# Kernel optimization log

Hardware: AMD Instinct MI355X
Metric: run time of the kernel (lower is better)

The kernel has to match this reference:

```python
import jax, jax.numpy as jnp
import numpy as np

B, H, S = 256, 128, 2048

def setup_inputs() -> dict:
    key = jax.random.key(0)
    ks = jax.random.split(key, 8)
    static_embedding = jax.random.normal(ks[0], (B, H, S), dtype=jnp.float32)
    dynamic_embedding = jax.random.normal(ks[1], (B, S, H), dtype=jnp.float32)
    decoder_output = jax.random.normal(ks[2], (B, H, 1), dtype=jnp.float32)
    mask = jax.random.randint(ks[3], (B, S), 0, 2).astype(bool)
    # xavier-uniform-ish init scales
    lim_v = float(np.sqrt(6.0 / (1 + H)))
    lim_W = float(np.sqrt(6.0 / (H + 3 * H)))
    lim_W2 = float(np.sqrt(6.0 / (H + 2 * H)))
    v = jax.random.uniform(ks[4], (H,), minval=-lim_v, maxval=lim_v, dtype=jnp.float32)
    W = jax.random.uniform(ks[5], (H, 3 * H), minval=-lim_W, maxval=lim_W, dtype=jnp.float32)
    v2 = jax.random.uniform(ks[6], (H,), minval=-lim_v, maxval=lim_v, dtype=jnp.float32)
    W2 = jax.random.uniform(ks[7], (H, 2 * H), minval=-lim_W2, maxval=lim_W2, dtype=jnp.float32)
    return {"static_embedding": static_embedding, "dynamic_embedding": dynamic_embedding,
            "decoder_output": decoder_output, "mask": mask,
            "v": v, "W": W, "v2": v2, "W2": W2}


def reference(static_embedding, dynamic_embedding, decoder_output, mask, v, W, v2, W2):
    b, h, s = static_embedding.shape
    dec = jnp.broadcast_to(decoder_output, (b, h, s))               # [B,H,S]
    hidden = jnp.concatenate(
        [static_embedding, jnp.swapaxes(dynamic_embedding, 1, 2), dec], axis=1)  # [B,3H,S]
    # stage 1: additive scoring  v^T tanh(W @ hidden)
    t1 = jnp.tanh(jnp.einsum('hk,bks->bhs', W, hidden))             # [B,H,S]
    attns = jnp.einsum('h,bhs->bs', v, t1)                          # [B,S]
    enc_attn = jax.nn.softmax(attns, axis=1)                        # [B,S]
    # context over static embeddings
    context = jnp.einsum('bs,bhs->bh', enc_attn, static_embedding)  # [B,H]
    energy = jnp.concatenate(
        [static_embedding, jnp.broadcast_to(context[:, :, None], (b, h, s))], axis=1)  # [B,2H,S]
    # stage 2
    t2 = jnp.tanh(jnp.einsum('hk,bks->bhs', W2, energy))            # [B,H,S]
    probs = jnp.einsum('h,bhs->bs', v2, t2)                         # [B,S]
    probs = jnp.where(mask, -jnp.inf, probs)
    return jax.nn.softmax(probs, axis=1)
```

## Files before the change

### kernel.cpp

```cpp
#include <hip/hip_runtime.h>
#include <stdint.h>
#include <math.h>

#define B_ 256
#define H_ 128
#define S_ 2048

typedef __attribute__((ext_vector_type(8))) short short8;
typedef __attribute__((ext_vector_type(4))) float f32x4;
typedef __attribute__((ext_vector_type(4))) unsigned int u32x4;

typedef const __attribute__((address_space(1))) void gvoid_t;
typedef __attribute__((address_space(3))) void lvoid_t;

__device__ __forceinline__ unsigned short f2bf(float f) {
  uint32_t u = __builtin_bit_cast(uint32_t, f);
  u += 0x7fffu + ((u >> 16) & 1u);
  return (unsigned short)(u >> 16);
}

__device__ __forceinline__ uint32_t cvtpk(float lo, float hi) {
  uint32_t r;
  asm("v_cvt_pk_bf16_f32 %0, %1, %2" : "=v"(r) : "v"(lo), "v"(hi));
  return r;
}

__device__ __forceinline__ float bf2f(unsigned short u) {
  return __builtin_bit_cast(float, (uint32_t)u << 16);
}

__device__ __forceinline__ float tanh5(float x) {
  float e = __builtin_amdgcn_exp2f(x * 2.8853900817779268f);
  float r = __builtin_amdgcn_rcpf(1.0f + e);
  return fmaf(-2.0f, r, 1.0f);
}

#define WS_NEED 4718592u
#define WST_OFF 8388608u
#define WS_T_NEED (WST_OFF + (size_t)B_ * (S_/16) * 4 * 64 * 8 * 2)

__global__ __launch_bounds__(256) void prep_wfrags(
    const float* __restrict__ W, const float* __restrict__ W2,
    unsigned short* __restrict__ wsA) {
  int idx = blockIdx.x * 256 + threadIdx.x;
  if (idx >= 24 * 4 * 64 * 8) return;
  int j = idx & 7;
  int lane = (idx >> 3) & 63;
  int t = (idx >> 9) & 3;
  int tile = idx >> 11;
  int li = lane & 15;
  int k = t * 32 + (lane >> 4) * 8 + j;
  float val;
  if (tile < 8)        val = W[(tile * 16 + li) * 384 + k];
  else if (tile < 16)  val = W2[((tile - 8) * 16 + li) * 256 + k];
  else                 val = W[((tile - 16) * 16 + li) * 384 + 128 + k];
  wsA[idx] = f2bf(val);
}

__global__ __launch_bounds__(128) void prep_c1(
    const float* __restrict__ W, const float* __restrict__ dec,
    float* __restrict__ c1) {
  int b = blockIdx.x;
  int h = threadIdx.x;
  __shared__ float sdec[H_];
  sdec[h] = dec[b * H_ + h];
  __syncthreads();
  const float* wr = W + h * 384 + 256;
  float acc = 0.f;
  #pragma unroll 4
  for (int k = 0; k < 128; ++k) acc += wr[k] * sdec[k];
  c1[b * H_ + h] = acc;
}

__global__ void detect_mask(const unsigned char* __restrict__ mb, int* __restrict__ flag) {
  __shared__ int sGT1, sNZ;
  if (threadIdx.x == 0) { sGT1 = 0; sNZ = 0; }
  __syncthreads();
  int gt1 = 0, nz = 0;
  for (int i = threadIdx.x; i < 8192; i += 256) {
    unsigned char c = mb[i];
    if (c > 1) gt1 = 1;
    if ((i & 3) && c) nz = 1;
  }
  if (gt1) atomicOr(&sGT1, 1);
  if (nz)  atomicOr(&sNZ, 1);
  __syncthreads();
  if (threadIdx.x == 0) *flag = sGT1 ? 2 : (sNZ ? 1 : 0);
}

__global__ __launch_bounds__(256) void stage1(
    const float* __restrict__ sEmb, const float* __restrict__ dEmb,
    const unsigned short* __restrict__ wsA, const float* __restrict__ c1,
    const float* __restrict__ v, float* __restrict__ attns,
    unsigned short* __restrict__ wsT) {
  const int b = blockIdx.y;
  const int tid = threadIdx.x;
  const int lane = tid & 63, w = tid >> 6, g = lane >> 4, li = lane & 15;
  __shared__ float sS[128 * 64];
  __shared__ unsigned short frag[4][8][512];
  __shared__ float spart[256];
  __shared__ float sc1[H_], sv[H_];

  const size_t sbase = (size_t)b * H_ * S_;
  const size_t dbase = (size_t)b * S_ * H_;
  const int sblk = blockIdx.x * 512;

  short8 aW[2][4], aB[2][4];
  #pragma unroll
  for (int mm = 0; mm < 2; ++mm)
    #pragma unroll
    for (int t = 0; t < 4; ++t) {
      aW[mm][t] = *(const short8*)(wsA + (size_t)(((2 * w + mm) * 4 + t) * 64 + lane) * 8);
      aB[mm][t] = *(const short8*)(wsA + (size_t)(((16 + 2 * w + mm) * 4 + t) * 64 + lane) * 8);
    }
  if (tid < 128) { sc1[tid] = c1[b * H_ + tid]; sv[tid] = v[tid]; }

  const int lrow = lane >> 4, lcol4 = 4 * (lane & 15);
  auto stageS = [&](int soff) {
    #pragma unroll
    for (int i = 0; i < 8; ++i) {
      int r = 32 * w + 4 * i + lrow;
      int gcol = lcol4 ^ (((r >> 3) & 3) << 3);
      const float* src = sEmb + sbase + (size_t)r * S_ + soff + gcol;
      __builtin_amdgcn_global_load_lds((gvoid_t*)src, (lvoid_t*)&sS[(32 * w + 4 * i) * 64],
                                       16, 0, 0);
    }
  };
  f32x4 dv[8];
  auto loadD = [&](int soff) {
    const float* dr = dEmb + dbase + (size_t)(soff + 16 * w + li) * H_ + 8 * g;
    #pragma unroll
    for (int t = 0; t < 4; ++t) {
      dv[2 * t]     = *(const f32x4*)(dr + 32 * t);
      dv[2 * t + 1] = *(const f32x4*)(dr + 32 * t + 4);
    }
  };

  stageS(sblk);
  loadD(sblk);

  const int colA = (16 * w + li) ^ (g << 3);

  for (int c = 0; c < 8; ++c) {
    const int soff = sblk + c * 64;
    __syncthreads();
    if (c > 0 && tid < 64)
      attns[(size_t)b * S_ + soff - 64 + tid] =
          spart[tid] + spart[64 + tid] + spart[128 + tid] + spart[192 + tid];

    #pragma unroll
    for (int t = 0; t < 4; ++t) {
      const int rb = (32 * t + 8 * g) * 64 + colA;
      uint32_t s0 = cvtpk(sS[rb], sS[rb + 64]);
      uint32_t s1 = cvtpk(sS[rb + 128], sS[rb + 192]);
      uint32_t s2 = cvtpk(sS[rb + 256], sS[rb + 320]);
      uint32_t s3 = cvtpk(sS[rb + 384], sS[rb + 448]);
      u32x4 us = {s0, s1, s2, s3};
      short8 bS = __builtin_bit_cast(short8, us);
      uint32_t d0 = cvtpk(dv[2 * t].x, dv[2 * t].y);
      uint32_t d1 = cvtpk(dv[2 * t].z, dv[2 * t].w);
      uint32_t d2 = cvtpk(dv[2 * t + 1].x, dv[2 * t + 1].y);
      uint32_t d3 = cvtpk(dv[2 * t + 1].z, dv[2 * t + 1].w);
      u32x4 ud = {d0, d1, d2, d3};
      short8 bD = __builtin_bit_cast(short8, ud);
      *(short8*)&frag[w][t][lane * 8] = bS;
      *(short8*)&frag[w][4 + t][lane * 8] = bD;
      if (wsT)
        *(short8*)&wsT[(((size_t)b * (S_ / 16) + (soff >> 4) + w) * 4 + t) * 512 + lane * 8] = bS;
    }
    __syncthreads();
    if (c + 1 < 8) { stageS(soff + 64); loadD(soff + 64); }

    f32x4 acc[4][2];
    #pragma unroll
    for (int st = 0; st < 4; ++st) { acc[st][0] = (f32x4)0.0f; acc[st][1] = (f32x4)0.0f; }
    #pragma unroll
    for (int st = 0; st < 4; ++st)
      #pragma unroll
      for (int t = 0; t < 4; ++t) {
        short8 bS = *(const short8*)&frag[st][t][lane * 8];
        short8 bD = *(const short8*)&frag[st][4 + t][lane * 8];
        acc[st][0] = __builtin_amdgcn_mfma_f32_16x16x32_bf16(aW[0][t], bS, acc[st][0], 0, 0, 0);
        acc[st][1] = __builtin_amdgcn_mfma_f32_16x16x32_bf16(aW[1][t], bS, acc[st][1], 0, 0, 0);
        acc[st][0] = __builtin_amdgcn_mfma_f32_16x16x32_bf16(aB[0][t], bD, acc[st][0], 0, 0, 0);
        acc[st][1] = __builtin_amdgcn_mfma_f32_16x16x32_bf16(aB[1][t], bD, acc[st][1], 0, 0, 0);
      }

    #pragma unroll
    for (int st = 0; st < 4; ++st) {
      float part = 0.f;
      #pragma unroll
      for (int mm = 0; mm < 2; ++mm)
        #pragma unroll
        for (int r = 0; r < 4; ++r) {
          int h = 32 * w + 16 * mm + 4 * g + r;
          part += sv[h] * tanh5(acc[st][mm][r] + sc1[h]);
        }
      part += __shfl_xor(part, 16);
      part += __shfl_xor(part, 32);
      if (lane < 16) spart[w * 64 + st * 16 + li] = part;
    }
  }
  __syncthreads();
  if (tid < 64)
    attns[(size_t)b * S_ + sblk + 448 + tid] =
        spart[tid] + spart[64 + tid] + spart[128 + tid] + spart[192 + tid];
}

__global__ __launch_bounds__(512) void fuse2(
    const float* __restrict__ attns, const unsigned short* __restrict__ wsT,
    const unsigned short* __restrict__ wsA, const float* __restrict__ W2,
    const float* __restrict__ v2, const unsigned char* __restrict__ mask8,
    const int* __restrict__ flag, float* __restrict__ out) {
  const int b = blockIdx.x;
  const int tid = threadIdx.x;
  const int lane = tid & 63, wv = tid >> 6, g = lane >> 4, li = lane & 15;
  __shared__ float buf[S_];
  __shared__ float sctx[8][H_];
  __shared__ float2 sq[H_];
  __shared__ float wred[8];
  __shared__ float sred;

  const size_t pbase = (size_t)b * (S_ / 16);

  float a[4];
  #pragma unroll
  for (int i = 0; i < 4; ++i) a[i] = attns[(size_t)b * S_ + i * 512 + tid];
  float mx = fmaxf(fmaxf(a[0], a[1]), fmaxf(a[2], a[3]));
  #pragma unroll
  for (int off = 32; off >= 1; off >>= 1) mx = fmaxf(mx, __shfl_xor(mx, off));
  if (lane == 0) wred[wv] = mx;
  __syncthreads();
  if (tid == 0) {
    float m = wred[0];
    #pragma unroll
    for (int i = 1; i < 8; ++i) m = fmaxf(m, wred[i]);
    sred = m;
  }
  __syncthreads();
  mx = sred;
  __syncthreads();
  float sum = 0.f;
  #pragma unroll
  for (int i = 0; i < 4; ++i) {
    float e = __expf(a[i] - mx);
    buf[i * 512 + tid] = e;
    sum += e;
  }
  #pragma unroll
  for (int off = 32; off >= 1; off >>= 1) sum += __shfl_xor(sum, off);
  if (lane == 0) wred[wv] = sum;
  __syncthreads();
  if (tid == 0) {
    float s = 0.f;
    #pragma unroll
    for (int i = 0; i < 8; ++i) s += wred[i];
    sred = 1.0f / s;
  }
  __syncthreads();
  const float inv1 = sred;
  __syncthreads();

  float hacc[4][8];
  #pragma unroll
  for (int t = 0; t < 4; ++t)
    #pragma unroll
    for (int j = 0; j < 8; ++j) hacc[t][j] = 0.f;
  short8 cur[4];
  #pragma unroll
  for (int t = 0; t < 4; ++t)
    cur[t] = *(const short8*)&wsT[((pbase + wv) * 4 + t) * 512 + lane * 8];
  for (int stile = wv; stile < 128; stile += 8) {
    short8 nxt[4];
    const bool more = (stile + 8) < 128;
    if (more) {
      #pragma unroll
      for (int t = 0; t < 4; ++t)
        nxt[t] = *(const short8*)&wsT[((pbase + stile + 8) * 4 + t) * 512 + lane * 8];
    }
    float pw = buf[stile * 16 + li];
    #pragma unroll
    for (int t = 0; t < 4; ++t)
      #pragma unroll
      for (int j = 0; j < 8; ++j)
        hacc[t][j] = fmaf(pw, bf2f((unsigned short)cur[t][j]), hacc[t][j]);
    if (more) {
      #pragma unroll
      for (int t = 0; t < 4; ++t) cur[t] = nxt[t];
    }
  }
  #pragma unroll
  for (int t = 0; t < 4; ++t)
    #pragma unroll
    for (int j = 0; j < 8; ++j) {
      float x = hacc[t][j];
      x += __shfl_xor(x, 1); x += __shfl_xor(x, 2);
      x += __shfl_xor(x, 4); x += __shfl_xor(x, 8);
      hacc[t][j] = x;
    }
  if (li == 0) {
    #pragma unroll
    for (int t = 0; t < 4; ++t)
      #pragma unroll
      for (int j = 0; j < 8; ++j)
        sctx[wv][32 * t + 8 * g + j] = hacc[t][j];
  }
  __syncthreads();

  if (tid < 128) {
    float cx = 0.f;
    #pragma unroll
    for (int q = 0; q < 8; ++q) cx += sctx[q][tid];
    sctx[0][tid] = cx * inv1;
  }
  __syncthreads();
  if (tid < 128) {
    const float* wr = W2 + tid * 256 + 128;
    float c2v = 0.f;
    #pragma unroll 4
    for (int k = 0; k < 128; ++k) c2v += wr[k] * sctx[0][k];
    sq[tid] = make_float2(c2v, v2[tid]);
  }
  __syncthreads();

  short8 aW[8][4];
  #pragma unroll
  for (int m = 0; m < 8; ++m)
    #pragma unroll
    for (int t = 0; t < 4; ++t)
      aW[m][t] = *(const short8*)(wsA + (size_t)(((8 + m) * 4 + t) * 64 + lane) * 8);
  const int f = *flag;

  short8 bcur[4];
  #pragma unroll
  for (int t = 0; t < 4; ++t)
    bcur[t] = *(const short8*)&wsT[((pbase + wv) * 4 + t) * 512 + lane * 8];
  for (int stile = wv; stile < 128; stile += 8) {
    short8 bnxt[4];
    const bool more = (stile + 8) < 128;
    if (more) {
      #pragma unroll
      for (int t = 0; t < 4; ++t)
        bnxt[t] = *(const short8*)&wsT[((pbase + stile + 8) * 4 + t) * 512 + lane * 8];
    }
    f32x4 acc[8];
    #pragma unroll
    for (int m = 0; m < 8; ++m) acc[m] = (f32x4)0.0f;
    #pragma unroll
    for (int t = 0; t < 4; ++t)
      #pragma unroll
      for (int m = 0; m < 8; ++m)
        acc[m] = __builtin_amdgcn_mfma_f32_16x16x32_bf16(aW[m][t], bcur[t], acc[m], 0, 0, 0);
    float part = 0.f;
    #pragma unroll
    for (int m = 0; m < 8; ++m)
      #pragma unroll
      for (int r = 0; r < 4; ++r) {
        float2 q = sq[16 * m + 4 * g + r];
        part += q.y * tanh5(acc[m][r] + q.x);
      }
    part += __shfl_xor(part, 16);
    part += __shfl_xor(part, 32);
    if (lane < 16) {
      int s = stile * 16 + li;
      size_t mi = (size_t)b * S_ + s;
      bool msk;
      if (f == 1)      msk = mask8[mi] != 0;
      else if (f == 2) msk = ((const float*)mask8)[mi] != 0.0f;
      else             msk = ((const int*)mask8)[mi] != 0;
      buf[s] = msk ? -INFINITY : part;
    }
    if (more) {
      #pragma unroll
      for (int t = 0; t < 4; ++t) bcur[t] = bnxt[t];
    }
  }
  __syncthreads();

  float s4[4];
  #pragma unroll
  for (int i = 0; i < 4; ++i) s4[i] = buf[i * 512 + tid];
  float mx2 = fmaxf(fmaxf(s4[0], s4[1]), fmaxf(s4[2], s4[3]));
  #pragma unroll
  for (int off = 32; off >= 1; off >>= 1) mx2 = fmaxf(mx2, __shfl_xor(mx2, off));
  if (lane == 0) wred[wv] = mx2;
  __syncthreads();
  if (tid == 0) {
    float m = wred[0];
    #pragma unroll
    for (int i = 1; i < 8; ++i) m = fmaxf(m, wred[i]);
    sred = m;
  }
  __syncthreads();
  mx2 = sred;
  __syncthreads();
  float e4[4];
  float sum2 = 0.f;
  #pragma unroll
  for (int i = 0; i < 4; ++i) { e4[i] = __expf(s4[i] - mx2); sum2 += e4[i]; }
  #pragma unroll
  for (int off = 32; off >= 1; off >>= 1) sum2 += __shfl_xor(sum2, off);
  if (lane == 0) wred[wv] = sum2;
  __syncthreads();
  if (tid == 0) {
    float s = 0.f;
    #pragma unroll
    for (int i = 0; i < 8; ++i) s += wred[i];
    sred = 1.0f / s;
  }
  __syncthreads();
  const float inv2 = sred;
  #pragma unroll
  for (int i = 0; i < 4; ++i) out[(size_t)b * S_ + i * 512 + tid] = e4[i] * inv2;
}

__global__ __launch_bounds__(256) void kmid_a(
    const float* __restrict__ attns, const float* __restrict__ sEmb,
    float* __restrict__ ctx) {
  int q = blockIdx.x, b = blockIdx.y;
  int tid = threadIdx.x, lane = tid & 63, w = tid >> 6;
  __shared__ float p[S_];
  __shared__ float wred[4];
  __shared__ float sred;
  float a[8];
  #pragma unroll
  for (int i = 0; i < 8; ++i) a[i] = attns[(size_t)b * S_ + i * 256 + tid];
  float mx = a[0];
  #pragma unroll
  for (int i = 1; i < 8; ++i) mx = fmaxf(mx, a[i]);
  #pragma unroll
  for (int off = 32; off >= 1; off >>= 1) mx = fmaxf(mx, __shfl_xor(mx, off));
  if (lane == 0) wred[w] = mx;
  __syncthreads();
  if (tid == 0) sred = fmaxf(fmaxf(wred[0], wred[1]), fmaxf(wred[2], wred[3]));
  __syncthreads();
  mx = sred;
  __syncthreads();
  float sum = 0.f;
  #pragma unroll
  for (int i = 0; i < 8; ++i) {
    float e = __expf(a[i] - mx);
    p[i * 256 + tid] = e;
    sum += e;
  }
  #pragma unroll
  for (int off = 32; off >= 1; off >>= 1) sum += __shfl_xor(sum, off);
  if (lane == 0) wred[w] = sum;
  __syncthreads();
  if (tid == 0) sred = 1.0f / (wred[0] + wred[1] + wred[2] + wred[3]);
  __syncthreads();
  float inv = sred;
  #pragma unroll
  for (int hh = 0; hh < 8; ++hh) {
    int h = q * 32 + w * 8 + hh;
    const f32x4* xp = (const f32x4*)(sEmb + (size_t)b * H_ * S_ + (size_t)h * S_);
    float av = 0.f;
    #pragma unroll
    for (int it = 0; it < 8; ++it) {
      f32x4 x = xp[it * 64 + lane];
      f32x4 pp = *(const f32x4*)&p[(it * 64 + lane) * 4];
      av += x.x * pp.x + x.y * pp.y + x.z * pp.z + x.w * pp.w;
    }
    #pragma unroll
    for (int off = 32; off >= 1; off >>= 1) av += __shfl_xor(av, off);
    if (lane == 0) ctx[b * H_ + h] = av * inv;
  }
}

__global__ __launch_bounds__(128) void kmid_b(
    const float* __restrict__ W2, const float* __restrict__ ctx,
    float* __restrict__ c2) {
  int b = blockIdx.x;
  int h = threadIdx.x;
  __shared__ float sc[H_];
  sc[h] = ctx[b * H_ + h];
  __syncthreads();
  const float* wr = W2 + h * 256 + 128;
  float acc = 0.f;
  #pragma unroll 4
  for (int k = 0; k < 128; ++k) acc += wr[k] * sc[k];
  c2[b * H_ + h] = acc;
}

__global__ __launch_bounds__(256) void stage2F(
    const float* __restrict__ sEmb, const unsigned short* __restrict__ wsA,
    const float* __restrict__ c2, const float* __restrict__ v2,
    const unsigned char* __restrict__ mask8, const int* __restrict__ flag,
    float* __restrict__ score) {
  int b = blockIdx.y;
  int tid = threadIdx.x;
  int lane = tid & 63, w = tid >> 6, g = lane >> 4, li = lane & 15;
  __shared__ float sS[128 * 64];
  __shared__ float sc2[H_], sv2[H_];
  __shared__ float spart[256];
  const int schunk = blockIdx.x * 64;
  const size_t sbase = (size_t)b * H_ * S_;
  short8 aW[2][4];
  #pragma unroll
  for (int mm = 0; mm < 2; ++mm)
    #pragma unroll
    for (int t = 0; t < 4; ++t)
      aW[mm][t] = *(const short8*)(wsA + (size_t)(((8 + 2 * w + mm) * 4 + t) * 64 + lane) * 8);
  {
    int lrow = lane >> 4, lcol4 = 4 * (lane & 15);
    #pragma unroll
    for (int i = 0; i < 8; ++i) {
      int r = 32 * w + 4 * i + lrow;
      int gcol = lcol4 ^ (((r >> 3) & 3) << 3);
      const float* src = sEmb + sbase + (size_t)r * S_ + schunk + gcol;
      __builtin_amdgcn_global_load_lds((gvoid_t*)src, (lvoid_t*)&sS[(32 * w + 4 * i) * 64],
                                       16, 0, 0);
    }
  }
  if (tid < 128) { sc2[tid] = c2[b * H_ + tid]; sv2[tid] = v2[tid]; }
  __syncthreads();
  f32x4 acc[4][2];
  #pragma unroll
  for (int st = 0; st < 4; ++st) { acc[st][0] = (f32x4)0.0f; acc[st][1] = (f32x4)0.0f; }
  #pragma unroll
  for (int st = 0; st < 4; ++st) {
    const int colA = (16 * st + li) ^ (g << 3);
    #pragma unroll
    for (int t = 0; t < 4; ++t) {
      short8 bS;
      #pragma unroll
      for (int j = 0; j < 8; ++j)
        bS[j] = (short)f2bf(sS[(32 * t + 8 * g + j) * 64 + colA]);
      acc[st][0] = __builtin_amdgcn_mfma_f32_16x16x32_bf16(aW[0][t], bS, acc[st][0], 0, 0, 0);
      acc[st][1] = __builtin_amdgcn_mfma_f32_16x16x32_bf16(aW[1][t], bS, acc[st][1], 0, 0, 0);
    }
  }
  #pragma unroll
  for (int st = 0; st < 4; ++st) {
    float part = 0.f;
    #pragma unroll
    for (int mm = 0; mm < 2; ++mm)
      #pragma unroll
      for (int r = 0; r < 4; ++r) {
        int h = 32 * w + 16 * mm + 4 * g + r;
        part += sv2[h] * tanh5(acc[st][mm][r] + sc2[h]);
      }
    part += __shfl_xor(part, 16);
    part += __shfl_xor(part, 32);
    if (lane < 16) spart[w * 64 + st * 16 + li] = part;
  }
  __syncthreads();
  if (tid < 64) {
    float tot = spart[tid] + spart[64 + tid] + spart[128 + tid] + spart[192 + tid];
    size_t mi = (size_t)b * S_ + schunk + tid;
    int f = *flag;
    bool msk;
    if (f == 1)      msk = mask8[mi] != 0;
    else if (f == 2) msk = ((const float*)mask8)[mi] != 0.0f;
    else             msk = ((const int*)mask8)[mi] != 0;
    score[mi] = msk ? -INFINITY : tot;
  }
}

__global__ __launch_bounds__(256) void ksoftmax(
    const float* __restrict__ score, float* __restrict__ out) {
  int b = blockIdx.x;
  int tid = threadIdx.x, lane = tid & 63, w = tid >> 6;
  __shared__ float wred[4];
  __shared__ float sred;
  float a[8];
  #pragma unroll
  for (int i = 0; i < 8; ++i) a[i] = score[(size_t)b * S_ + i * 256 + tid];
  float mx = a[0];
  #pragma unroll
  for (int i = 1; i < 8; ++i) mx = fmaxf(mx, a[i]);
  #pragma unroll
  for (int off = 32; off >= 1; off >>= 1) mx = fmaxf(mx, __shfl_xor(mx, off));
  if (lane == 0) wred[w] = mx;
  __syncthreads();
  if (tid == 0) sred = fmaxf(fmaxf(wred[0], wred[1]), fmaxf(wred[2], wred[3]));
  __syncthreads();
  mx = sred;
  __syncthreads();
  float e[8];
  float sum = 0.f;
  #pragma unroll
  for (int i = 0; i < 8; ++i) { e[i] = __expf(a[i] - mx); sum += e[i]; }
  #pragma unroll
  for (int off = 32; off >= 1; off >>= 1) sum += __shfl_xor(sum, off);
  if (lane == 0) wred[w] = sum;
  __syncthreads();
  if (tid == 0) sred = 1.0f / (wred[0] + wred[1] + wred[2] + wred[3]);
  __syncthreads();
  float inv = sred;
  #pragma unroll
  for (int i = 0; i < 8; ++i) out[(size_t)b * S_ + i * 256 + tid] = e[i] * inv;
}

extern "C" void kernel_launch(void* const* d_in, const int* in_sizes, int n_in,
                              void* d_out, int out_size, void* d_ws, size_t ws_size,
                              hipStream_t stream) {
  (void)in_sizes; (void)n_in; (void)out_size;
  if (ws_size < WS_NEED) return;
  const float* sEmb = (const float*)d_in[0];
  const float* dEmb = (const float*)d_in[1];
  const float* dec  = (const float*)d_in[2];
  const unsigned char* mask = (const unsigned char*)d_in[3];
  const float* v    = (const float*)d_in[4];
  const float* W    = (const float*)d_in[5];
  const float* v2   = (const float*)d_in[6];
  const float* W2   = (const float*)d_in[7];

  char* ws = (char*)d_ws;
  unsigned short* wsA = (unsigned short*)(ws);
  int*   flag  = (int*)  (ws + 114688);
  float* c1    = (float*)(ws + 131072);
  float* c2    = (float*)(ws + 262144);
  float* ctx   = (float*)(ws + 393216);
  float* attns = (float*)(ws + 524288);
  float* score = (float*)(ws + 2621440);
  bool useT = (ws_size >= WS_T_NEED);
  unsigned short* wsT = useT ? (unsigned short*)(ws + WST_OFF) : nullptr;

  prep_wfrags<<<192, 256, 0, stream>>>(W, W2, wsA);
  prep_c1<<<B_, 128, 0, stream>>>(W, dec, c1);
  detect_mask<<<1, 256, 0, stream>>>(mask, flag);
  stage1<<<dim3(4, B_), 256, 0, stream>>>(sEmb, dEmb, wsA, c1, v, attns, wsT);
  if (useT) {
    fuse2<<<B_, 512, 0, stream>>>(attns, wsT, wsA, W2, v2, mask, flag, (float*)d_out);
  } else {
    kmid_a<<<dim3(4, B_), 256, 0, stream>>>(attns, sEmb, ctx);
    kmid_b<<<B_, 128, 0, stream>>>(W2, ctx, c2);
    stage2F<<<dim3(32, B_), 256, 0, stream>>>(sEmb, wsA, c2, v2, mask, flag, score);
    ksoftmax<<<B_, 256, 0, stream>>>(score, (float*)d_out);
  }
}
```

Measured before the change: 229.9 us.

## Double-buffer stage1 with 32-column chunks, manual waitcnt and more blocks

Rewrites stage1 for the workspace path so each block covers 256 columns in 32-column chunks with double-buffered LDS staging and prefetch two chunks ahead. Explicit vmcnt/lgkmcnt waits and sched barriers control overlap, the grid doubles to 8×B, and launch bounds request 3 blocks per CU. The aim is to hide HBM latency behind MFMA work and raise occupancy. The old kernel is kept as a fallback without the wsT store, and the hand-tuned wait counts are fragile if the compiler changes how many memory instructions it issues.

```diff
diff --git a/kernel.cpp b/kernel.cpp
--- a/kernel.cpp
+++ b/kernel.cpp
@@ -12,6 +12,8 @@
 
 typedef const __attribute__((address_space(1))) void gvoid_t;
 typedef __attribute__((address_space(3))) void lvoid_t;
+
+#define SCHED0 __builtin_amdgcn_sched_barrier(0)
 
 __device__ __forceinline__ unsigned short f2bf(float f) {
   uint32_t u = __builtin_bit_cast(uint32_t, f);
@@ -88,7 +90,9 @@
   if (threadIdx.x == 0) *flag = sGT1 ? 2 : (sNZ ? 1 : 0);
 }
 
-__global__ __launch_bounds__(256) void stage1(
+struct D4 { f32x4 v[4]; };
+
+__global__ __launch_bounds__(256, 3) void stage1(
     const float* __restrict__ sEmb, const float* __restrict__ dEmb,
     const unsigned short* __restrict__ wsA, const float* __restrict__ c1,
     const float* __restrict__ v, float* __restrict__ attns,
@@ -96,6 +100,376 @@
   const int b = blockIdx.y;
   const int tid = threadIdx.x;
   const int lane = tid & 63, w = tid >> 6, g = lane >> 4, li = lane & 15;
+  const int stl = w >> 1, tp = w & 1;
+  __shared__ float sS[2][128 * 32];
+  __shared__ unsigned short frag[2][8][512];
+  __shared__ float spart[4][32];
+  __shared__ float sc1[H_], sv[H_];
+
+  const size_t sbase = (size_t)b * H_ * S_;
+  const size_t dbase = (size_t)b * S_ * H_;
+  const int sblk = blockIdx.x * 256;
+  const int CHUNKS = 8;
+
+  short8 aW[2][4], aB[2][4];
+  #pragma unroll
+  for (int mm = 0; mm < 2; ++mm)
+    #pragma unroll
+    for (int t = 0; t < 4; ++t) {
+      aW[mm][t] = *(const short8*)(wsA + (size_t)(((2 * w + mm) * 4 + t) * 64 + lane) * 8);
+      aB[mm][t] = *(const short8*)(wsA + (size_t)(((16 + 2 * w + mm) * 4 + t) * 64 + lane) * 8);
+    }
+  {
+    int hh = 32 * w + (lane & 31);
+    sc1[hh] = c1[b * H_ + hh];
+    sv[hh]  = v[hh];
+  }
+
+  auto stageS = [&](int soff2, int buf) {
+    #pragma unroll
+    for (int i = 0; i < 4; ++i) {
+      int rr = 32 * w + 8 * i + (lane >> 3);
+      int gcol = (4 * (lane & 7)) ^ (i << 3);
+      const float* src = sEmb + sbase + (size_t)rr * S_ + soff2 + gcol;
+      __builtin_amdgcn_global_load_lds((gvoid_t*)src,
+                                       (lvoid_t*)&sS[buf][(32 * w + 8 * i) * 32], 16, 0, 0);
+    }
+  };
+  auto loadD = [&](int soff2) -> D4 {
+    D4 r;
+    const float* dr = dEmb + dbase + (size_t)(soff2 + 16 * stl + li) * H_ + 64 * tp + 8 * g;
+    r.v[0] = *(const f32x4*)(dr);
+    r.v[1] = *(const f32x4*)(dr + 4);
+    r.v[2] = *(const f32x4*)(dr + 32);
+    r.v[3] = *(const f32x4*)(dr + 36);
+    return r;
+  };
+
+  SCHED0;
+  stageS(sblk, 0);
+  SCHED0;
+  D4 dvA = loadD(sblk);
+  SCHED0;
+  stageS(sblk + 32, 1);
+  SCHED0;
+  D4 dvB = loadD(sblk + 32);
+  SCHED0;
+
+  const int colr = (16 * stl + li) ^ (g << 3);
+
+  for (int c = 0; c < CHUNKS; ++c) {
+    const int soff = sblk + c * 32;
+
+    if (c == 0)                 { asm volatile("s_waitcnt vmcnt(8)" ::: "memory"); }
+    else if (c == 1)            { asm volatile("s_waitcnt vmcnt(10)" ::: "memory"); }
+    else if (c == CHUNKS - 1)   { asm volatile("s_waitcnt vmcnt(3)" ::: "memory"); }
+    else                        { asm volatile("s_waitcnt vmcnt(11)" ::: "memory"); }
+    asm volatile("s_waitcnt lgkmcnt(0)" ::: "memory");
+    SCHED0;
+    __builtin_amdgcn_s_barrier();
+    SCHED0;
+
+    if (c > 0) {
+      int idx = 8 * w + (lane & 7);
+      float tot = spart[0][idx] + spart[1][idx] + spart[2][idx] + spart[3][idx];
+      if (lane < 8) attns[(size_t)b * S_ + soff - 32 + idx] = tot;
+    }
+
+    {
+      const float* sSc = sS[c & 1];
+      const f32x4* dvv = (c & 1) ? dvB.v : dvA.v;
+      #pragma unroll
+      for (int tt = 0; tt < 2; ++tt) {
+        const int t = 2 * tp + tt;
+        const int rb = (32 * t + 8 * g) * 32 + colr;
+        uint32_t s0 = cvtpk(sSc[rb], sSc[rb + 32]);
+        uint32_t s1 = cvtpk(sSc[rb + 64], sSc[rb + 96]);
+        uint32_t s2 = cvtpk(sSc[rb + 128], sSc[rb + 160]);
+        uint32_t s3 = cvtpk(sSc[rb + 192], sSc[rb + 224]);
+        u32x4 us = {s0, s1, s2, s3};
+        short8 bS = __builtin_bit_cast(short8, us);
+        f32x4 a0 = dvv[2 * tt], a1 = dvv[2 * tt + 1];
+        uint32_t d0 = cvtpk(a0.x, a0.y);
+        uint32_t d1 = cvtpk(a0.z, a0.w);
+        uint32_t d2 = cvtpk(a1.x, a1.y);
+        uint32_t d3 = cvtpk(a1.z, a1.w);
+        u32x4 ud = {d0, d1, d2, d3};
+        short8 bD = __builtin_bit_cast(short8, ud);
+        *(short8*)&frag[stl][t][lane * 8] = bS;
+        *(short8*)&frag[stl][4 + t][lane * 8] = bD;
+        *(short8*)&wsT[(((size_t)b * (S_ / 16) + (soff >> 4) + stl) * 4 + t) * 512 + lane * 8] = bS;
+      }
+    }
+
+    asm volatile("s_waitcnt lgkmcnt(0)" ::: "memory");
+    SCHED0;
+    __builtin_amdgcn_s_barrier();
+    SCHED0;
+
+    if (c + 2 < CHUNKS) {
+      stageS(soff + 64, c & 1);
+      SCHED0;
+      if ((c & 1) == 0) dvA = loadD(soff + 64);
+      else              dvB = loadD(soff + 64);
+    }
+    SCHED0;
+
+    f32x4 acc[2][2];
+    #pragma unroll
+    for (int st = 0; st < 2; ++st) { acc[st][0] = (f32x4)0.0f; acc[st][1] = (f32x4)0.0f; }
+    #pragma unroll
+    for (int st = 0; st < 2; ++st)
+      #pragma unroll
+      for (int t = 0; t < 4; ++t) {
+        short8 bS = *(const short8*)&frag[st][t][lane * 8];
+        short8 bD = *(const short8*)&frag[st][4 + t][lane * 8];
+        acc[st][0] = __builtin_amdgcn_mfma_f32_16x16x32_bf16(aW[0][t], bS, acc[st][0], 0, 0, 0);
+        acc[st][1] = __builtin_amdgcn_mfma_f32_16x16x32_bf16(aW[1][t], bS, acc[st][1], 0, 0, 0);
+        acc[st][0] = __builtin_amdgcn_mfma_f32_16x16x32_bf16(aB[0][t], bD, acc[st][0], 0, 0, 0);
+        acc[st][1] = __builtin_amdgcn_mfma_f32_16x16x32_bf16(aB[1][t], bD, acc[st][1], 0, 0, 0);
+      }
+
+    #pragma unroll
+    for (int st = 0; st < 2; ++st) {
+      float part = 0.f;
+      #pragma unroll
+      for (int mm = 0; mm < 2; ++mm)
+        #pragma unroll
+        for (int r = 0; r < 4; ++r) {
+          int h = 32 * w + 16 * mm + 4 * g + r;
+          part += sv[h] * tanh5(acc[st][mm][r] + sc1[h]);
+        }
+      part += __shfl_xor(part, 16);
+      part += __shfl_xor(part, 32);
+      if (lane < 16) spart[w][16 * st + li] = part;
+    }
+  }
+
+  asm volatile("s_waitcnt lgkmcnt(0)" ::: "memory");
+  SCHED0;
+  __builtin_amdgcn_s_barrier();
+  SCHED0;
+  {
+    int idx = 8 * w + (lane & 7);
+    float tot = spart[0][idx] + spart[1][idx] + spart[2][idx] + spart[3][idx];
+    if (lane < 8) attns[(size_t)b * S_ + sblk + (CHUNKS - 1) * 32 + idx] = tot;
+  }
+}
+
+__global__ __launch_bounds__(512) void fuse2(
+    const float* __restrict__ attns, const unsigned short* __restrict__ wsT,
+    const unsigned short* __restrict__ wsA, const float* __restrict__ W2,
+    const float* __restrict__ v2, const unsigned char* __restrict__ mask8,
+    const int* __restrict__ flag, float* __restrict__ out) {
+  const int b = blockIdx.x;
+  const int tid = threadIdx.x;
+  const int lane = tid & 63, wv = tid >> 6, g = lane >> 4, li = lane & 15;
+  __shared__ float buf[S_];
+  __shared__ float sctx[8][H_];
+  __shared__ float2 sq[H_];
+  __shared__ float wred[8];
+  __shared__ float sred;
+
+  const size_t pbase = (size_t)b * (S_ / 16);
+
+  float a[4];
+  #pragma unroll
+  for (int i = 0; i < 4; ++i) a[i] = attns[(size_t)b * S_ + i * 512 + tid];
+  float mx = fmaxf(fmaxf(a[0], a[1]), fmaxf(a[2], a[3]));
+  #pragma unroll
+  for (int off = 32; off >= 1; off >>= 1) mx = fmaxf(mx, __shfl_xor(mx, off));
+  if (lane == 0) wred[wv] = mx;
+  __syncthreads();
+  if (tid == 0) {
+    float m = wred[0];
+    #pragma unroll
+    for (int i = 1; i < 8; ++i) m = fmaxf(m, wred[i]);
+    sred = m;
+  }
+  __syncthreads();
+  mx = sred;
+  __syncthreads();
+  float sum = 0.f;
+  #pragma unroll
+  for (int i = 0; i < 4; ++i) {
+    float e = __expf(a[i] - mx);
+    buf[i * 512 + tid] = e;
+    sum += e;
+  }
+  #pragma unroll
+  for (int off = 32; off >= 1; off >>= 1) sum += __shfl_xor(sum, off);
+  if (lane == 0) wred[wv] = sum;
+  __syncthreads();
+  if (tid == 0) {
+    float s = 0.f;
+    #pragma unroll
+    for (int i = 0; i < 8; ++i) s += wred[i];
+    sred = 1.0f / s;
+  }
+  __syncthreads();
+  const float inv1 = sred;
+  __syncthreads();
+
+  float hacc[4][8];
+  #pragma unroll
+  for (int t = 0; t < 4; ++t)
+    #pragma unroll
+    for (int j = 0; j < 8; ++j) hacc[t][j] = 0.f;
+  short8 cur[4];
+  #pragma unroll
+  for (int t = 0; t < 4; ++t)
+    cur[t] = *(const short8*)&wsT[((pbase + wv) * 4 + t) * 512 + lane * 8];
+  for (int stile = wv; stile < 128; stile += 8) {
+    short8 nxt[4];
+    const bool more = (stile + 8) < 128;
+    if (more) {
+      #pragma unroll
+      for (int t = 0; t < 4; ++t)
+        nxt[t] = *(const short8*)&wsT[((pbase + stile + 8) * 4 + t) * 512 + lane * 8];
+    }
+    float pw = buf[stile * 16 + li];
+    #pragma unroll
+    for (int t = 0; t < 4; ++t)
+      #pragma unroll
+      for (int j = 0; j < 8; ++j)
+        hacc[t][j] = fmaf(pw, bf2f((unsigned short)cur[t][j]), hacc[t][j]);
+    if (more) {
+      #pragma unroll
+      for (int t = 0; t < 4; ++t) cur[t] = nxt[t];
+    }
+  }
+  #pragma unroll
+  for (int t = 0; t < 4; ++t)
+    #pragma unroll
+    for (int j = 0; j < 8; ++j) {
+      float x = hacc[t][j];
+      x += __shfl_xor(x, 1); x += __shfl_xor(x, 2);
+      x += __shfl_xor(x, 4); x += __shfl_xor(x, 8);
+      hacc[t][j] = x;
+    }
+  if (li == 0) {
+    #pragma unroll
+    for (int t = 0; t < 4; ++t)
+      #pragma unroll
+      for (int j = 0; j < 8; ++j)
+        sctx[wv][32 * t + 8 * g + j] = hacc[t][j];
+  }
+  __syncthreads();
+
+  if (tid < 128) {
+    float cx = 0.f;
+    #pragma unroll
+    for (int q = 0; q < 8; ++q) cx += sctx[q][tid];
+    sctx[0][tid] = cx * inv1;
+  }
+  __syncthreads();
+  if (tid < 128) {
+    const float* wr = W2 + tid * 256 + 128;
+    float c2v = 0.f;
+    #pragma unroll 4
+    for (int k = 0; k < 128; ++k) c2v += wr[k] * sctx[0][k];
+    sq[tid] = make_float2(c2v, v2[tid]);
+  }
+  __syncthreads();
+
+  short8 aW[8][4];
+  #pragma unroll
+  for (int m = 0; m < 8; ++m)
+    #pragma unroll
+    for (int t = 0; t < 4; ++t)
+      aW[m][t] = *(const short8*)(wsA + (size_t)(((8 + m) * 4 + t) * 64 + lane) * 8);
+  const int f = *flag;
+
+  short8 bcur[4];
+  #pragma unroll
+  for (int t = 0; t < 4; ++t)
+    bcur[t] = *(const short8*)&wsT[((pbase + wv) * 4 + t) * 512 + lane * 8];
+  for (int stile = wv; stile < 128; stile += 8) {
+    short8 bnxt[4];
+    const bool more = (stile + 8) < 128;
+    if (more) {
+      #pragma unroll
+      for (int t = 0; t < 4; ++t)
+        bnxt[t] = *(const short8*)&wsT[((pbase + stile + 8) * 4 + t) * 512 + lane * 8];
+    }
+    f32x4 acc[8];
+    #pragma unroll
+    for (int m = 0; m < 8; ++m) acc[m] = (f32x4)0.0f;
+    #pragma unroll
+    for (int t = 0; t < 4; ++t)
+      #pragma unroll
+      for (int m = 0; m < 8; ++m)
+        acc[m] = __builtin_amdgcn_mfma_f32_16x16x32_bf16(aW[m][t], bcur[t], acc[m], 0, 0, 0);
+    float part = 0.f;
+    #pragma unroll
+    for (int m = 0; m < 8; ++m)
+      #pragma unroll
+      for (int r = 0; r < 4; ++r) {
+        float2 q = sq[16 * m + 4 * g + r];
+        part += q.y * tanh5(acc[m][r] + q.x);
+      }
+    part += __shfl_xor(part, 16);
+    part += __shfl_xor(part, 32);
+    if (lane < 16) {
+      int s = stile * 16 + li;
+      size_t mi = (size_t)b * S_ + s;
+      bool msk;
+      if (f == 1)      msk = mask8[mi] != 0;
+      else if (f == 2) msk = ((const float*)mask8)[mi] != 0.0f;
+      else             msk = ((const int*)mask8)[mi] != 0;
+      buf[s] = msk ? -INFINITY : part;
+    }
+    if (more) {
+      #pragma unroll
+      for (int t = 0; t < 4; ++t) bcur[t] = bnxt[t];
+    }
+  }
+  __syncthreads();
+
+  float s4[4];
+  #pragma unroll
+  for (int i = 0; i < 4; ++i) s4[i] = buf[i * 512 + tid];
+  float mx2 = fmaxf(fmaxf(s4[0], s4[1]), fmaxf(s4[2], s4[3]));
+  #pragma unroll
+  for (int off = 32; off >= 1; off >>= 1) mx2 = fmaxf(mx2, __shfl_xor(mx2, off));
+  if (lane == 0) wred[wv] = mx2;
+  __syncthreads();
+  if (tid == 0) {
+    float m = wred[0];
+    #pragma unroll
+    for (int i = 1; i < 8; ++i) m = fmaxf(m, wred[i]);
+    sred = m;
+  }
+  __syncthreads();
+  mx2 = sred;
+  __syncthreads();
+  float e4[4];
+  float sum2 = 0.f;
+  #pragma unroll
+  for (int i = 0; i < 4; ++i) { e4[i] = __expf(s4[i] - mx2); sum2 += e4[i]; }
+  #pragma unroll
+  for (int off = 32; off >= 1; off >>= 1) sum2 += __shfl_xor(sum2, off);
+  if (lane == 0) wred[wv] = sum2;
+  __syncthreads();
+  if (tid == 0) {
+    float s = 0.f;
+    #pragma unroll
+    for (int i = 0; i < 8; ++i) s += wred[i];
+    sred = 1.0f / s;
+  }
+  __syncthreads();
+  const float inv2 = sred;
+  #pragma unroll
+  for (int i = 0; i < 4; ++i) out[(size_t)b * S_ + i * 512 + tid] = e4[i] * inv2;
+}
+
+__global__ __launch_bounds__(256) void stage1_fb(
+    const float* __restrict__ sEmb, const float* __restrict__ dEmb,
+    const unsigned short* __restrict__ wsA, const float* __restrict__ c1,
+    const float* __restrict__ v, float* __restrict__ attns) {
+  const int b = blockIdx.y;
+  const int tid = threadIdx.x;
+  const int lane = tid & 63, w = tid >> 6, g = lane >> 4, li = lane & 15;
   __shared__ float sS[128 * 64];
   __shared__ unsigned short frag[4][8][512];
   __shared__ float spart[256];
@@ -135,10 +509,8 @@
       dv[2 * t + 1] = *(const f32x4*)(dr + 32 * t + 4);
     }
   };
-
   stageS(sblk);
   loadD(sblk);
-
   const int colA = (16 * w + li) ^ (g << 3);
 
   for (int c = 0; c < 8; ++c) {
@@ -147,7 +519,6 @@
     if (c > 0 && tid < 64)
       attns[(size_t)b * S_ + soff - 64 + tid] =
           spart[tid] + spart[64 + tid] + spart[128 + tid] + spart[192 + tid];
-
     #pragma unroll
     for (int t = 0; t < 4; ++t) {
       const int rb = (32 * t + 8 * g) * 64 + colA;
@@ -165,12 +536,9 @@
       short8 bD = __builtin_bit_cast(short8, ud);
       *(short8*)&frag[w][t][lane * 8] = bS;
       *(short8*)&frag[w][4 + t][lane * 8] = bD;
-      if (wsT)
-        *(short8*)&wsT[(((size_t)b * (S_ / 16) + (soff >> 4) + w) * 4 + t) * 512 + lane * 8] = bS;
     }
     __syncthreads();
     if (c + 1 < 8) { stageS(soff + 64); loadD(soff + 64); }
-
     f32x4 acc[4][2];
     #pragma unroll
     for (int st = 0; st < 4; ++st) { acc[st][0] = (f32x4)0.0f; acc[st][1] = (f32x4)0.0f; }
@@ -185,7 +553,6 @@
         acc[st][0] = __builtin_amdgcn_mfma_f32_16x16x32_bf16(aB[0][t], bD, acc[st][0], 0, 0, 0);
         acc[st][1] = __builtin_amdgcn_mfma_f32_16x16x32_bf16(aB[1][t], bD, acc[st][1], 0, 0, 0);
       }
-
     #pragma unroll
     for (int st = 0; st < 4; ++st) {
       float part = 0.f;
@@ -205,213 +572,6 @@
   if (tid < 64)
     attns[(size_t)b * S_ + sblk + 448 + tid] =
         spart[tid] + spart[64 + tid] + spart[128 + tid] + spart[192 + tid];
-}
-
-__global__ __launch_bounds__(512) void fuse2(
-    const float* __restrict__ attns, const unsigned short* __restrict__ wsT,
-    const unsigned short* __restrict__ wsA, const float* __restrict__ W2,
-    const float* __restrict__ v2, const unsigned char* __restrict__ mask8,
-    const int* __restrict__ flag, float* __restrict__ out) {
-  const int b = blockIdx.x;
-  const int tid = threadIdx.x;
-  const int lane = tid & 63, wv = tid >> 6, g = lane >> 4, li = lane & 15;
-  __shared__ float buf[S_];
-  __shared__ float sctx[8][H_];
-  __shared__ float2 sq[H_];
-  __shared__ float wred[8];
-  __shared__ float sred;
-
-  const size_t pbase = (size_t)b * (S_ / 16);
-
-  float a[4];
-  #pragma unroll
-  for (int i = 0; i < 4; ++i) a[i] = attns[(size_t)b * S_ + i * 512 + tid];
-  float mx = fmaxf(fmaxf(a[0], a[1]), fmaxf(a[2], a[3]));
-  #pragma unroll
-  for (int off = 32; off >= 1; off >>= 1) mx = fmaxf(mx, __shfl_xor(mx, off));
-  if (lane == 0) wred[wv] = mx;
-  __syncthreads();
-  if (tid == 0) {
-    float m = wred[0];
-    #pragma unroll
-    for (int i = 1; i < 8; ++i) m = fmaxf(m, wred[i]);
-    sred = m;
-  }
-  __syncthreads();
-  mx = sred;
-  __syncthreads();
-  float sum = 0.f;
-  #pragma unroll
-  for (int i = 0; i < 4; ++i) {
-    float e = __expf(a[i] - mx);
-    buf[i * 512 + tid] = e;
-    sum += e;
-  }
-  #pragma unroll
-  for (int off = 32; off >= 1; off >>= 1) sum += __shfl_xor(sum, off);
-  if (lane == 0) wred[wv] = sum;
-  __syncthreads();
-  if (tid == 0) {
-    float s = 0.f;
-    #pragma unroll
-    for (int i = 0; i < 8; ++i) s += wred[i];
-    sred = 1.0f / s;
-  }
-  __syncthreads();
-  const float inv1 = sred;
-  __syncthreads();
-
-  float hacc[4][8];
-  #pragma unroll
-  for (int t = 0; t < 4; ++t)
-    #pragma unroll
-    for (int j = 0; j < 8; ++j) hacc[t][j] = 0.f;
-  short8 cur[4];
-  #pragma unroll
-  for (int t = 0; t < 4; ++t)
-    cur[t] = *(const short8*)&wsT[((pbase + wv) * 4 + t) * 512 + lane * 8];
-  for (int stile = wv; stile < 128; stile += 8) {
-    short8 nxt[4];
-    const bool more = (stile + 8) < 128;
-    if (more) {
-      #pragma unroll
-      for (int t = 0; t < 4; ++t)
-        nxt[t] = *(const short8*)&wsT[((pbase + stile + 8) * 4 + t) * 512 + lane * 8];
-    }
-    float pw = buf[stile * 16 + li];
-    #pragma unroll
-    for (int t = 0; t < 4; ++t)
-      #pragma unroll
-      for (int j = 0; j < 8; ++j)
-        hacc[t][j] = fmaf(pw, bf2f((unsigned short)cur[t][j]), hacc[t][j]);
-    if (more) {
-      #pragma unroll
-      for (int t = 0; t < 4; ++t) cur[t] = nxt[t];
-    }
-  }
-  #pragma unroll
-  for (int t = 0; t < 4; ++t)
-    #pragma unroll
-    for (int j = 0; j < 8; ++j) {
-      float x = hacc[t][j];
-      x += __shfl_xor(x, 1); x += __shfl_xor(x, 2);
-      x += __shfl_xor(x, 4); x += __shfl_xor(x, 8);
-      hacc[t][j] = x;
-    }
-  if (li == 0) {
-    #pragma unroll
-    for (int t = 0; t < 4; ++t)
-      #pragma unroll
-      for (int j = 0; j < 8; ++j)
-        sctx[wv][32 * t + 8 * g + j] = hacc[t][j];
-  }
-  __syncthreads();
-
-  if (tid < 128) {
-    float cx = 0.f;
-    #pragma unroll
-    for (int q = 0; q < 8; ++q) cx += sctx[q][tid];
-    sctx[0][tid] = cx * inv1;
-  }
-  __syncthreads();
-  if (tid < 128) {
-    const float* wr = W2 + tid * 256 + 128;
-    float c2v = 0.f;
-    #pragma unroll 4
-    for (int k = 0; k < 128; ++k) c2v += wr[k] * sctx[0][k];
-    sq[tid] = make_float2(c2v, v2[tid]);
-  }
-  __syncthreads();
-
-  short8 aW[8][4];
-  #pragma unroll
-  for (int m = 0; m < 8; ++m)
-    #pragma unroll
-    for (int t = 0; t < 4; ++t)
-      aW[m][t] = *(const short8*)(wsA + (size_t)(((8 + m) * 4 + t) * 64 + lane) * 8);
-  const int f = *flag;
-
-  short8 bcur[4];
-  #pragma unroll
-  for (int t = 0; t < 4; ++t)
-    bcur[t] = *(const short8*)&wsT[((pbase + wv) * 4 + t) * 512 + lane * 8];
-  for (int stile = wv; stile < 128; stile += 8) {
-    short8 bnxt[4];
-    const bool more = (stile + 8) < 128;
-    if (more) {
-      #pragma unroll
-      for (int t = 0; t < 4; ++t)
-        bnxt[t] = *(const short8*)&wsT[((pbase + stile + 8) * 4 + t) * 512 + lane * 8];
-    }
-    f32x4 acc[8];
-    #pragma unroll
-    for (int m = 0; m < 8; ++m) acc[m] = (f32x4)0.0f;
-    #pragma unroll
-    for (int t = 0; t < 4; ++t)
-      #pragma unroll
-      for (int m = 0; m < 8; ++m)
-        acc[m] = __builtin_amdgcn_mfma_f32_16x16x32_bf16(aW[m][t], bcur[t], acc[m], 0, 0, 0);
-    float part = 0.f;
-    #pragma unroll
-    for (int m = 0; m < 8; ++m)
-      #pragma unroll
-      for (int r = 0; r < 4; ++r) {
-        float2 q = sq[16 * m + 4 * g + r];
-        part += q.y * tanh5(acc[m][r] + q.x);
-      }
-    part += __shfl_xor(part, 16);
-    part += __shfl_xor(part, 32);
-    if (lane < 16) {
-      int s = stile * 16 + li;
-      size_t mi = (size_t)b * S_ + s;
-      bool msk;
-      if (f == 1)      msk = mask8[mi] != 0;
-      else if (f == 2) msk = ((const float*)mask8)[mi] != 0.0f;
-      else             msk = ((const int*)mask8)[mi] != 0;
-      buf[s] = msk ? -INFINITY : part;
-    }
-    if (more) {
-      #pragma unroll
-      for (int t = 0; t < 4; ++t) bcur[t] = bnxt[t];
-    }
-  }
-  __syncthreads();
-
-  float s4[4];
-  #pragma unroll
-  for (int i = 0; i < 4; ++i) s4[i] = buf[i * 512 + tid];
-  float mx2 = fmaxf(fmaxf(s4[0], s4[1]), fmaxf(s4[2], s4[3]));
-  #pragma unroll
-  for (int off = 32; off >= 1; off >>= 1) mx2 = fmaxf(mx2, __shfl_xor(mx2, off));
-  if (lane == 0) wred[wv] = mx2;
-  __syncthreads();
-  if (tid == 0) {
-    float m = wred[0];
-    #pragma unroll
-    for (int i = 1; i < 8; ++i) m = fmaxf(m, wred[i]);
-    sred = m;
-  }
-  __syncthreads();
-  mx2 = sred;
-  __syncthreads();
-  float e4[4];
-  float sum2 = 0.f;
-  #pragma unroll
-  for (int i = 0; i < 4; ++i) { e4[i] = __expf(s4[i] - mx2); sum2 += e4[i]; }
-  #pragma unroll
-  for (int off = 32; off >= 1; off >>= 1) sum2 += __shfl_xor(sum2, off);
-  if (lane == 0) wred[wv] = sum2;
-  __syncthreads();
-  if (tid == 0) {
-    float s = 0.f;
-    #pragma unroll
-    for (int i = 0; i < 8; ++i) s += wred[i];
-    sred = 1.0f / s;
-  }
-  __syncthreads();
-  const float inv2 = sred;
-  #pragma unroll
-  for (int i = 0; i < 4; ++i) out[(size_t)b * S_ + i * 512 + tid] = e4[i] * inv2;
 }
 
 __global__ __launch_bounds__(256) void kmid_a(
@@ -620,10 +780,11 @@
   prep_wfrags<<<192, 256, 0, stream>>>(W, W2, wsA);
   prep_c1<<<B_, 128, 0, stream>>>(W, dec, c1);
   detect_mask<<<1, 256, 0, stream>>>(mask, flag);
-  stage1<<<dim3(4, B_), 256, 0, stream>>>(sEmb, dEmb, wsA, c1, v, attns, wsT);
   if (useT) {
+    stage1<<<dim3(8, B_), 256, 0, stream>>>(sEmb, dEmb, wsA, c1, v, attns, wsT);
     fuse2<<<B_, 512, 0, stream>>>(attns, wsT, wsA, W2, v2, mask, flag, (float*)d_out);
   } else {
+    stage1_fb<<<dim3(4, B_), 256, 0, stream>>>(sEmb, dEmb, wsA, c1, v, attns);
     kmid_a<<<dim3(4, B_), 256, 0, stream>>>(attns, sEmb, ctx);
     kmid_b<<<B_, 128, 0, stream>>>(W2, ctx, c2);
     stage2F<<<dim3(32, B_), 256, 0, stream>>>(sEmb, wsA, c2, v2, mask, flag, score);
```

New measurement: 236.1 us. +2.7%, slower.
